# Optimization experiments

Measured on AMD Instinct MI355X. Metric: run time of the kernel, lower is better.

Reference implementation:

```python
import jax, jax.numpy as jnp
import numpy as np

DIM = 64   # flow dimension
HID = 8    # hidden_dim=[8]
B = 131072 # batch of samples


def setup_inputs() -> dict:
    key = jax.random.key(0)
    ks = jax.random.split(key, 6)
    L = DIM - 1  # number of per-dim MLPs (layers[0..L-1], layer l has fan-in l+1)
    lim = float(np.sqrt(0.5))
    x = jax.random.normal(ks[0], (B, DIM), jnp.float32)
    initial_param = jax.random.uniform(ks[1], (2,), jnp.float32, -lim, lim)
    # Ragged Linear(fan_in=l+1, 8) weights stacked into padded [L, HID, L];
    # entries beyond column l are masked to zero in reference().
    fan_in = np.arange(1, DIM).astype(np.float32)          # (L,)
    bnd1 = (1.0 / np.sqrt(fan_in))[:, None, None]          # torch Linear default init bound
    W1 = jax.random.uniform(ks[2], (L, HID, L), jnp.float32, -1.0, 1.0) * bnd1
    b1 = jax.random.uniform(ks[3], (L, HID), jnp.float32, -1.0, 1.0) * bnd1[:, :, 0]
    bnd2 = 1.0 / np.sqrt(HID)
    W2 = jax.random.uniform(ks[4], (L, 2, HID), jnp.float32, -bnd2, bnd2)
    b2 = jax.random.uniform(ks[5], (L, 2), jnp.float32, -bnd2, bnd2)
    return {"x": x, "initial_param": initial_param, "W1": W1, "b1": b1, "W2": W2, "b2": b2}


def reference(x, initial_param, W1, b1, W2, b2):
    B_, D = x.shape
    L = W1.shape[0]  # D - 1
    # mask[l, d] = 1 iff d <= l  ->  layer l sees exactly x[:, :l+1]
    mask = jnp.tril(jnp.ones((L, L), x.dtype))
    W1m = W1 * mask[:, None, :]
    # all dim-1 tiny MLPs fused into two batched contractions
    h = jnp.tanh(jnp.einsum('bd,lhd->blh', x[:, :L], W1m) + b1)   # [B, L, HID]
    out = jnp.einsum('blh,loh->blo', h, W2) + b2                   # [B, L, 2]
    mu0 = jnp.broadcast_to(initial_param[0], (B_, 1)).astype(x.dtype)
    al0 = jnp.broadcast_to(initial_param[1], (B_, 1)).astype(x.dtype)
    mu = jnp.concatenate([mu0, out[:, :, 0]], axis=1)              # [B, D]
    alpha = jnp.concatenate([al0, out[:, :, 1]], axis=1)           # [B, D]
    z = x * jnp.exp(alpha) + mu
    log_det = jnp.sum(alpha, axis=1)
    return z, log_det
```

## Files before the change

### kernel.cpp

```cpp
#include <hip/hip_runtime.h>
#include <hip/hip_cooperative_groups.h>


namespace cg = cooperative_groups;

#define DIMS 64
#define TPB  512
#define WAVES 8
#define SPW  16
#define GRID 1024

typedef __attribute__((ext_vector_type(8))) short short8;
typedef __attribute__((ext_vector_type(4))) float f32x4;
typedef __attribute__((ext_vector_type(4))) unsigned int uint4v;
typedef unsigned short ushort_t;
typedef unsigned int uint_t;

#if __has_builtin(__builtin_amdgcn_exp2f)
#define YSCALE 2.8853900817779268f
#define EXP2F(x) __builtin_amdgcn_exp2f(x)
#else
#define YSCALE 2.8853900817779268f
#define EXP2F(x) exp2f(x)
#endif
#define LOG2E 1.4426950408889634f
#define LN2   0.6931471805599453f

#define A_OFF 0
#define BLO_OFF 16384
#define BHI_OFF 32768
#define C_OFF 49152
#define WT_BYTES 55808
#define CDE_BYTES 6656
#define PREP_N (24576 + 1664)

#define XZ_OFF CDE_BYTES
#define LDS_BYTES (CDE_BYTES + WAVES * SPW * DIMS * 4)

__device__ __align__(16) unsigned char g_ws[WT_BYTES];

__device__ __forceinline__ uint_t pk2bf(float a, float b) {
#if __has_builtin(__builtin_amdgcn_cvt_pk_bf16_f32)
    typedef __attribute__((ext_vector_type(2))) __bf16 bf16x2;
    bf16x2 r = __builtin_amdgcn_cvt_pk_bf16_f32(a, b);
    return __builtin_bit_cast(uint_t, r);
#else
    uint_t ua = __float_as_uint(a); ua += 0x7FFFu + ((ua >> 16) & 1u);
    uint_t ub = __float_as_uint(b); ub += 0x7FFFu + ((ub >> 16) & 1u);
    return (ub & 0xFFFF0000u) | (ua >> 16);
#endif
}

__device__ __forceinline__ ushort_t f2bf(float f) {
    uint_t u = __float_as_uint(f);
    u += 0x7FFFu + ((u >> 16) & 1u);
    return (ushort_t)(u >> 16);
}

__device__ __forceinline__ int logrow(int p) {
    int n = p & 15;
    return (p >> 5) * 32 + (n >> 2) * 8 + ((p >> 4) & 1) * 4 + (n & 3);
}

__device__ __forceinline__ void prep_element(int i,
        const float* __restrict__ W1, const float* __restrict__ b1,
        const float* __restrict__ W2, const float* __restrict__ b2) {
    ushort_t* __restrict__ ws_u = (ushort_t*)g_ws;
    if (i < 8192) {
        int p = i >> 5, k = i & 31;
        int L = logrow(p), l = L >> 3, h = L & 7;
        float v = (k <= l) ? W1[(l * 8 + h) * 63 + k] * YSCALE : 0.0f;
        ws_u[i] = f2bf(v);
    } else if (i < 16384) {
        int r = i - 8192;
        int p = 256 + (r >> 5), k = r & 31;
        int L = logrow(p), l = L >> 3, h = L & 7;
        float v = (l < 63 && k <= l) ? W1[(l * 8 + h) * 63 + k] * YSCALE : 0.0f;
        ws_u[i] = f2bf(v);
    } else if (i < 24576) {
        int r = i - 16384;
        int p = 256 + (r >> 5), k = 32 + (r & 31);
        int L = logrow(p), l = L >> 3, h = L & 7;
        float v = (l < 63 && k <= l) ? W1[(l * 8 + h) * 63 + k] * YSCALE : 0.0f;
        ws_u[i] = f2bf(v);
    } else if (i < PREP_N) {
        int f = i - 24576;
        float* fws = (float*)(g_ws + C_OFF);
        float v = 0.0f;
        if (f < 1024) {
            int l = f >> 4, o = (f >> 3) & 1, h = f & 7;
            if (l < 63) {
                v = -2.0f * W2[(l * 2 + o) * 8 + h];
                if (o) v *= LOG2E;
            }
        } else if (f < 1536) {
            int p = f - 1024;
            int L = logrow(p), l = L >> 3, h = L & 7;
            if (l < 63) v = b1[l * 8 + h] * YSCALE;
        } else {
            int j = f - 1536, l = j >> 1, o = j & 1;
            if (l < 63) {
                float s = b2[l * 2 + o];
                #pragma unroll
                for (int h = 0; h < 8; ++h) s += W2[(l * 2 + o) * 8 + h];
                v = o ? s * LOG2E : s;
            }
        }
        fws[f] = v;
    }
}

__global__ void siaf_prep(const float* __restrict__ W1, const float* __restrict__ b1,
                          const float* __restrict__ W2, const float* __restrict__ b2) {
    prep_element(blockIdx.x * 256 + threadIdx.x, W1, b1, W2, b2);
}

__device__ __forceinline__ float sg(float t) {
    float e = EXP2F(t);
    return __builtin_amdgcn_rcpf(e + 1.0f);
}

__device__ __forceinline__ void x_stage(float* xzw, const float* __restrict__ x,
                                        int sbase, int s16, int quad, int lane) {
    #pragma unroll
    for (int g = 0; g < 4; ++g) {
        const float4 v = ((const float4*)(x + (size_t)sbase * DIMS))[g * 64 + lane];
        const int s_loc = 4 * g + quad;
        const int pc = (s16 ^ s_loc) & 15;
        *(float4*)(xzw + s_loc * 64 + pc * 4) = v;
    }
}

__device__ __forceinline__ void siaf_body(
        unsigned char* lds, const float* __restrict__ x,
        const float* __restrict__ ip, float* __restrict__ out, int nB,
        bool stage_x) {
    const int tid  = threadIdx.x;
    const int wv   = tid >> 6, lane = tid & 63;
    const int s16  = lane & 15, quad = lane >> 4;
    const int sbase = blockIdx.x * (WAVES * SPW) + wv * SPW;
    float* xzw = (float*)(lds + XZ_OFF) + wv * (SPW * DIMS);

    if (stage_x) x_stage(xzw, x, sbase, s16, quad, lane);
    const float ip0 = ip[0];
    const float ip1l2 = ip[1] * LOG2E;

    if (tid < CDE_BYTES / 16) {
        ((uint4*)lds)[tid] = ((const uint4*)(g_ws + C_OFF))[tid];
    }

    short8 bfr[2];
    #pragma unroll
    for (int kh = 0; kh < 2; ++kh) {
        const int c0 = kh * 8 + quad * 2;
        float4 va = *(const float4*)(xzw + s16 * 64 + ((c0 ^ s16) & 15) * 4);
        float4 vb = *(const float4*)(xzw + s16 * 64 + (((c0 + 1) ^ s16) & 15) * 4);
        uint4v u = {pk2bf(va.x, va.y), pk2bf(va.z, va.w),
                    pk2bf(vb.x, vb.y), pk2bf(vb.z, vb.w)};
        bfr[kh] = __builtin_bit_cast(short8, u);
    }

    __syncthreads();

    const float* w2f = (const float*)(lds);
    const float* b1f = (const float*)(lds + 4096);
    const float* b2f = (const float*)(lds + 6144);

    const ushort_t* gA   = (const ushort_t*)g_ws;
    const ushort_t* gBlo = (const ushort_t*)(g_ws + BLO_OFF);
    const ushort_t* gBhi = (const ushort_t*)(g_ws + BHI_OFF);
    const int fo = s16 * 32 + quad * 8;

    auto ldA = [&](int w, short8& a00, short8& a10, short8& a01, short8& a11) {
        if (w < 8) {
            const ushort_t* b = gA + w * 1024 + fo;
            a00 = *(const short8*)(b);
            a10 = *(const short8*)(b + 512);
        } else {
            const int off = (w - 8) * 1024 + fo;
            a00 = *(const short8*)(gBlo + off);
            a10 = *(const short8*)(gBlo + off + 512);
            a01 = *(const short8*)(gBhi + off);
            a11 = *(const short8*)(gBhi + off + 512);
        }
    };

    short8 A00[2], A10[2], A01[2] = {}, A11[2] = {};
    ldA(0, A00[0], A10[0], A01[0], A11[0]);

    float lsum = 0.0f;
    #pragma unroll
    for (int w = 0; w < 16; ++w) {
        const int cur = w & 1, nxt = cur ^ 1;
        if (w < 15) ldA(w + 1, A00[nxt], A10[nxt], A01[nxt], A11[nxt]);

        const float4 bi0 = *(const float4*)(b1f + w * 32 + quad * 4);
        const float4 bi1 = *(const float4*)(b1f + w * 32 + 16 + quad * 4);

        f32x4 aE = {bi0.x, bi0.y, bi0.z, bi0.w};
        f32x4 aO = {bi1.x, bi1.y, bi1.z, bi1.w};
        aE = __builtin_amdgcn_mfma_f32_16x16x32_bf16(A00[cur], bfr[0], aE, 0, 0, 0);
        aO = __builtin_amdgcn_mfma_f32_16x16x32_bf16(A10[cur], bfr[0], aO, 0, 0, 0);
        if (w >= 8) {
            aE = __builtin_amdgcn_mfma_f32_16x16x32_bf16(A01[cur], bfr[1], aE, 0, 0, 0);
            aO = __builtin_amdgcn_mfma_f32_16x16x32_bf16(A11[cur], bfr[1], aO, 0, 0, 0);
        }

        const float r0 = sg(aE[0]), r1 = sg(aE[1]), r2 = sg(aE[2]), r3 = sg(aE[3]);
        const float r4 = sg(aO[0]), r5 = sg(aO[1]), r6 = sg(aO[2]), r7 = sg(aO[3]);

        const int l = 4 * w + quad;
        const float4 m0 = *(const float4*)(w2f + l * 16);
        const float4 m1 = *(const float4*)(w2f + l * 16 + 4);
        const float4 a0 = *(const float4*)(w2f + l * 16 + 8);
        const float4 a1 = *(const float4*)(w2f + l * 16 + 12);
        const float2 bb = *(const float2*)(b2f + l * 2);

        float mu0 = bb.x, mu1 = m1.x * r4;
        mu0 = fmaf(m0.x, r0, mu0); mu1 = fmaf(m1.y, r5, mu1);
        mu0 = fmaf(m0.y, r1, mu0); mu1 = fmaf(m1.z, r6, mu1);
        mu0 = fmaf(m0.z, r2, mu0); mu1 = fmaf(m1.w, r7, mu1);
        mu0 = fmaf(m0.w, r3, mu0);
        float mu = mu0 + mu1;
        float al0 = bb.y, al1 = a1.x * r4;
        al0 = fmaf(a0.x, r0, al0); al1 = fmaf(a1.y, r5, al1);
        al0 = fmaf(a0.y, r1, al0); al1 = fmaf(a1.z, r6, al1);
        al0 = fmaf(a0.z, r2, al0); al1 = fmaf(a1.w, r7, al1);
        al0 = fmaf(a0.w, r3, al0);
        float alg = al0 + al1;

        int d = l + 1;
        if (w == 15) {
            const bool pad = (quad == 3);
            alg = pad ? ip1l2 : alg;
            mu  = pad ? ip0 : mu;
            d   = pad ? 0 : d;
        }
        float* pz = xzw + s16 * 64 + ((((d >> 2) ^ s16) & 15) << 2) + (d & 3);
        *pz = fmaf(*pz, EXP2F(alg), mu);
        lsum += alg;
    }

    #pragma unroll
    for (int g = 0; g < 4; ++g) {
        const int s_loc = 4 * g + quad;
        const int pc = (s16 ^ s_loc) & 15;
        const float4 v = *(const float4*)(xzw + s_loc * 64 + pc * 4);
        ((float4*)(out + (size_t)sbase * DIMS))[g * 64 + lane] = v;
    }

    {
        float v = lsum;
        int r1 = __builtin_amdgcn_ds_swizzle(__float_as_int(v), 0x401F);
        v += __int_as_float(r1);
        int r2 = __builtin_amdgcn_ds_bpermute((lane ^ 32) << 2, __float_as_int(v));
        v += __int_as_float(r2);
        if (quad == 0)
            out[(size_t)nB * DIMS + sbase + s16] = v * LN2;
    }
}

__global__ __launch_bounds__(TPB, 8) void siaf_main_fb(
        const float* __restrict__ x, const float* __restrict__ ip,
        float* __restrict__ out, int nB) {
    extern __shared__ unsigned char lds[];
    siaf_body(lds, x, ip, out, nB, true);
}

__global__ __launch_bounds__(TPB, 8) void siaf_fused(
        const float* __restrict__ x, const float* __restrict__ ip,
        const float* __restrict__ W1, const float* __restrict__ b1,
        const float* __restrict__ W2, const float* __restrict__ b2,
        float* __restrict__ out, int nB) {
    extern __shared__ unsigned char lds[];
    const int tid  = threadIdx.x;
    const int wv   = tid >> 6, lane = tid & 63;
    const int s16  = lane & 15, quad = lane >> 4;
    const int sbase = blockIdx.x * (WAVES * SPW) + wv * SPW;
    float* xzw = (float*)(lds + XZ_OFF) + wv * (SPW * DIMS);

    x_stage(xzw, x, sbase, s16, quad, lane);

    const int gi = blockIdx.x * TPB + tid;
    if (gi < PREP_N) prep_element(gi, W1, b1, W2, b2);

    __threadfence();
    cg::this_grid().sync();

    siaf_body(lds, x, ip, out, nB, false);
}

extern "C" void kernel_launch(void* const* d_in, const int* in_sizes, int n_in,
                              void* d_out, int out_size, void* d_ws, size_t ws_size,
                              hipStream_t stream) {
    const float* x  = (const float*)d_in[0];
    const float* ip = (const float*)d_in[1];
    const float* W1 = (const float*)d_in[2];
    const float* b1 = (const float*)d_in[3];
    const float* W2 = (const float*)d_in[4];
    const float* b2 = (const float*)d_in[5];
    float* out = (float*)d_out;
    (void)d_ws; (void)ws_size;

    const int nB = in_sizes[0] / DIMS;
    const int grid = nB / (WAVES * SPW);

    (void)hipFuncSetAttribute((const void*)siaf_fused,
                              hipFuncAttributeMaxDynamicSharedMemorySize, LDS_BYTES);
    (void)hipFuncSetAttribute((const void*)siaf_main_fb,
                              hipFuncAttributeMaxDynamicSharedMemorySize, LDS_BYTES);

    static int coop_ok = -1;
    if (coop_ok < 0) {
        int maxb = 0;
        hipError_t e = hipOccupancyMaxActiveBlocksPerMultiprocessor(
            &maxb, (const void*)siaf_fused, TPB, LDS_BYTES);
        coop_ok = (e == hipSuccess && maxb >= 4) ? 1 : 0;
    }

    bool launched = false;
    if (coop_ok == 1) {
        void* args[] = {(void*)&x, (void*)&ip, (void*)&W1, (void*)&b1,
                        (void*)&W2, (void*)&b2, (void*)&out, (void*)&nB};
        hipError_t e = hipLaunchCooperativeKernel(
            (const void*)siaf_fused, dim3(grid), dim3(TPB), args, LDS_BYTES, stream);
        if (e == hipSuccess) launched = true;
        else coop_ok = 0;
    }
    if (!launched) {
        siaf_prep<<<(PREP_N + 255) / 256, 256, 0, stream>>>(W1, b1, W2, b2);
        siaf_main_fb<<<grid, TPB, LDS_BYTES, stream>>>(x, ip, out, nB);
    }
}
```

Baseline: 113.6 us.

## Replace cooperative grid-sync fused kernel with separate prep and main launches

Removes the cooperative launch, whose grid-wide barrier sat between weight preprocessing and the main MFMA pass, and always runs a small prep kernel followed by the main kernel. The weight-tile prefetch is restructured to load two iterations ahead and to reuse the current buffer after its MFMAs issue. Launch bounds drop from 8 to 4 blocks per CU, which loosens the register limit. This trades the grid-sync cost and the x-load overlap with prep for one extra kernel launch and possibly lower occupancy.

```diff
diff --git a/kernel.cpp b/kernel.cpp
--- a/kernel.cpp
+++ b/kernel.cpp
@@ -1,14 +1,10 @@
 #include <hip/hip_runtime.h>
-#include <hip/hip_cooperative_groups.h>
-
-
-namespace cg = cooperative_groups;
+
 
 #define DIMS 64
 #define TPB  512
 #define WAVES 8
 #define SPW  16
-#define GRID 1024
 
 typedef __attribute__((ext_vector_type(8))) short short8;
 typedef __attribute__((ext_vector_type(4))) float f32x4;
@@ -62,10 +58,10 @@
     return (p >> 5) * 32 + (n >> 2) * 8 + ((p >> 4) & 1) * 4 + (n & 3);
 }
 
-__device__ __forceinline__ void prep_element(int i,
-        const float* __restrict__ W1, const float* __restrict__ b1,
-        const float* __restrict__ W2, const float* __restrict__ b2) {
+__global__ void siaf_prep(const float* __restrict__ W1, const float* __restrict__ b1,
+                          const float* __restrict__ W2, const float* __restrict__ b2) {
     ushort_t* __restrict__ ws_u = (ushort_t*)g_ws;
+    int i = blockIdx.x * 256 + threadIdx.x;
     if (i < 8192) {
         int p = i >> 5, k = i & 31;
         int L = logrow(p), l = L >> 3, h = L & 7;
@@ -110,18 +106,22 @@
     }
 }
 
-__global__ void siaf_prep(const float* __restrict__ W1, const float* __restrict__ b1,
-                          const float* __restrict__ W2, const float* __restrict__ b2) {
-    prep_element(blockIdx.x * 256 + threadIdx.x, W1, b1, W2, b2);
-}
-
 __device__ __forceinline__ float sg(float t) {
     float e = EXP2F(t);
     return __builtin_amdgcn_rcpf(e + 1.0f);
 }
 
-__device__ __forceinline__ void x_stage(float* xzw, const float* __restrict__ x,
-                                        int sbase, int s16, int quad, int lane) {
+__global__ __launch_bounds__(TPB, 4) void siaf_main(
+        const float* __restrict__ x, const float* __restrict__ ip,
+        float* __restrict__ out, int nB) {
+    extern __shared__ unsigned char lds[];
+
+    const int tid  = threadIdx.x;
+    const int wv   = tid >> 6, lane = tid & 63;
+    const int s16  = lane & 15, quad = lane >> 4;
+    const int sbase = blockIdx.x * (WAVES * SPW) + wv * SPW;
+    float* xzw = (float*)(lds + XZ_OFF) + wv * (SPW * DIMS);
+
     #pragma unroll
     for (int g = 0; g < 4; ++g) {
         const float4 v = ((const float4*)(x + (size_t)sbase * DIMS))[g * 64 + lane];
@@ -129,19 +129,6 @@
         const int pc = (s16 ^ s_loc) & 15;
         *(float4*)(xzw + s_loc * 64 + pc * 4) = v;
     }
-}
-
-__device__ __forceinline__ void siaf_body(
-        unsigned char* lds, const float* __restrict__ x,
-        const float* __restrict__ ip, float* __restrict__ out, int nB,
-        bool stage_x) {
-    const int tid  = threadIdx.x;
-    const int wv   = tid >> 6, lane = tid & 63;
-    const int s16  = lane & 15, quad = lane >> 4;
-    const int sbase = blockIdx.x * (WAVES * SPW) + wv * SPW;
-    float* xzw = (float*)(lds + XZ_OFF) + wv * (SPW * DIMS);
-
-    if (stage_x) x_stage(xzw, x, sbase, s16, quad, lane);
     const float ip0 = ip[0];
     const float ip1l2 = ip[1] * LOG2E;
 
@@ -187,12 +174,12 @@
 
     short8 A00[2], A10[2], A01[2] = {}, A11[2] = {};
     ldA(0, A00[0], A10[0], A01[0], A11[0]);
+    ldA(1, A00[1], A10[1], A01[1], A11[1]);
 
     float lsum = 0.0f;
     #pragma unroll
     for (int w = 0; w < 16; ++w) {
-        const int cur = w & 1, nxt = cur ^ 1;
-        if (w < 15) ldA(w + 1, A00[nxt], A10[nxt], A01[nxt], A11[nxt]);
+        const int cur = w & 1;
 
         const float4 bi0 = *(const float4*)(b1f + w * 32 + quad * 4);
         const float4 bi1 = *(const float4*)(b1f + w * 32 + 16 + quad * 4);
@@ -205,6 +192,8 @@
             aE = __builtin_amdgcn_mfma_f32_16x16x32_bf16(A01[cur], bfr[1], aE, 0, 0, 0);
             aO = __builtin_amdgcn_mfma_f32_16x16x32_bf16(A11[cur], bfr[1], aO, 0, 0, 0);
         }
+
+        if (w < 14) ldA(w + 2, A00[cur], A10[cur], A01[cur], A11[cur]);
 
         const float r0 = sg(aE[0]), r1 = sg(aE[1]), r2 = sg(aE[2]), r3 = sg(aE[3]);
         const float r4 = sg(aO[0]), r5 = sg(aO[1]), r6 = sg(aO[2]), r7 = sg(aO[3]);
@@ -260,36 +249,6 @@
     }
 }
 
-__global__ __launch_bounds__(TPB, 8) void siaf_main_fb(
-        const float* __restrict__ x, const float* __restrict__ ip,
-        float* __restrict__ out, int nB) {
-    extern __shared__ unsigned char lds[];
-    siaf_body(lds, x, ip, out, nB, true);
-}
-
-__global__ __launch_bounds__(TPB, 8) void siaf_fused(
-        const float* __restrict__ x, const float* __restrict__ ip,
-        const float* __restrict__ W1, const float* __restrict__ b1,
-        const float* __restrict__ W2, const float* __restrict__ b2,
-        float* __restrict__ out, int nB) {
-    extern __shared__ unsigned char lds[];
-    const int tid  = threadIdx.x;
-    const int wv   = tid >> 6, lane = tid & 63;
-    const int s16  = lane & 15, quad = lane >> 4;
-    const int sbase = blockIdx.x * (WAVES * SPW) + wv * SPW;
-    float* xzw = (float*)(lds + XZ_OFF) + wv * (SPW * DIMS);
-
-    x_stage(xzw, x, sbase, s16, quad, lane);
-
-    const int gi = blockIdx.x * TPB + tid;
-    if (gi < PREP_N) prep_element(gi, W1, b1, W2, b2);
-
-    __threadfence();
-    cg::this_grid().sync();
-
-    siaf_body(lds, x, ip, out, nB, false);
-}
-
 extern "C" void kernel_launch(void* const* d_in, const int* in_sizes, int n_in,
                               void* d_out, int out_size, void* d_ws, size_t ws_size,
                               hipStream_t stream) {
@@ -305,30 +264,9 @@
     const int nB = in_sizes[0] / DIMS;
     const int grid = nB / (WAVES * SPW);
 
-    (void)hipFuncSetAttribute((const void*)siaf_fused,
+    (void)hipFuncSetAttribute((const void*)siaf_main,
                               hipFuncAttributeMaxDynamicSharedMemorySize, LDS_BYTES);
-    (void)hipFuncSetAttribute((const void*)siaf_main_fb,
-                              hipFuncAttributeMaxDynamicSharedMemorySize, LDS_BYTES);
-
-    static int coop_ok = -1;
-    if (coop_ok < 0) {
-        int maxb = 0;
-        hipError_t e = hipOccupancyMaxActiveBlocksPerMultiprocessor(
-            &maxb, (const void*)siaf_fused, TPB, LDS_BYTES);
-        coop_ok = (e == hipSuccess && maxb >= 4) ? 1 : 0;
-    }
-
-    bool launched = false;
-    if (coop_ok == 1) {
-        void* args[] = {(void*)&x, (void*)&ip, (void*)&W1, (void*)&b1,
-                        (void*)&W2, (void*)&b2, (void*)&out, (void*)&nB};
-        hipError_t e = hipLaunchCooperativeKernel(
-            (const void*)siaf_fused, dim3(grid), dim3(TPB), args, LDS_BYTES, stream);
-        if (e == hipSuccess) launched = true;
-        else coop_ok = 0;
-    }
-    if (!launched) {
-        siaf_prep<<<(PREP_N + 255) / 256, 256, 0, stream>>>(W1, b1, W2, b2);
-        siaf_main_fb<<<grid, TPB, LDS_BYTES, stream>>>(x, ip, out, nB);
-    }
-}
+
+    siaf_prep<<<(PREP_N + 255) / 256, 256, 0, stream>>>(W1, b1, W2, b2);
+    siaf_main<<<grid, TPB, LDS_BYTES, stream>>>(x, ip, out, nB);
+}
```

Result: no change. 114.2 us (+0.5%).
